# Kernel tuning notes

Measured on AMD Instinct MI355X. Metric: run time of the kernel, lower is better.

The kernel has to match this reference:

```python
import jax, jax.numpy as jnp
import numpy as np

B, N, D, H = 2, 2048, 2048, 16
HD = D // H  # head_dim = 128
EPS = 1e-06

def rmsnorm(x, w, eps=EPS):
    xf = x.astype(jnp.float32)
    y = xf * jax.lax.rsqrt(jnp.mean(xf * xf, axis=-1, keepdims=True) + eps)
    return y.astype(x.dtype) * w

def rope_apply(x, freqs, num_heads):
    # x: [B, S, D]; freqs: [S, 1, HD//2, 2] = (cos, sin) of complex rotation
    b, s, d = x.shape
    hd = d // num_heads
    xr = x.reshape(b, s, num_heads, hd // 2, 2)
    x0, x1 = xr[..., 0], xr[..., 1]
    fr, fi = freqs[..., 0], freqs[..., 1]  # broadcast [S,1,HD//2] over heads
    out = jnp.stack([x0 * fr - x1 * fi, x0 * fi + x1 * fr], axis=-1)
    return out.reshape(b, s, d).astype(x.dtype)

def attention(q, k, v, num_heads):
    b, s, d = q.shape
    hd = d // num_heads
    qh = q.reshape(b, s, num_heads, hd).transpose(0, 2, 1, 3)  # b h s d
    kh = k.reshape(b, s, num_heads, hd).transpose(0, 2, 1, 3)
    vh = v.reshape(b, s, num_heads, hd).transpose(0, 2, 1, 3)
    scale = hd ** -0.5
    scores = jnp.einsum('bhqd,bhkd->bhqk', qh, kh) * scale
    probs = jax.nn.softmax(scores, axis=-1)
    out = jnp.einsum('bhqk,bhkd->bhqd', probs, vh)
    return out.transpose(0, 2, 1, 3).reshape(b, s, d)

def setup_inputs() -> dict:
    key = jax.random.key(0)
    ks = jax.random.split(key, 8)
    x = jax.random.normal(ks[0], (B, N, D), jnp.float32)
    # standard RoPE frequencies
    pos = jnp.arange(N, dtype=jnp.float32)
    inv = 1.0 / (10000.0 ** (jnp.arange(0, HD, 2, dtype=jnp.float32) / HD))
    ang = pos[:, None] * inv[None, :]  # [N, HD//2]
    freqs = jnp.stack([jnp.cos(ang), jnp.sin(ang)], axis=-1)[:, None, :, :]  # [N,1,HD//2,2]
    s = 0.02
    wq = jax.random.normal(ks[1], (D, D), jnp.float32) * s
    wk = jax.random.normal(ks[2], (D, D), jnp.float32) * s
    wv = jax.random.normal(ks[3], (D, D), jnp.float32) * s
    wo = jax.random.normal(ks[4], (D, D), jnp.float32) * s
    bq = jnp.zeros((D,), jnp.float32)
    bk = jnp.zeros((D,), jnp.float32)
    bv = jnp.zeros((D,), jnp.float32)
    bo = jnp.zeros((D,), jnp.float32)
    gq = jnp.ones((D,), jnp.float32)
    gk = jnp.ones((D,), jnp.float32)
    return {"x": x, "freqs": freqs, "wq": wq, "bq": bq, "wk": wk, "bk": bk,
            "wv": wv, "bv": bv, "wo": wo, "bo": bo, "gq": gq, "gk": gk}

def reference(x, freqs, wq, bq, wk, bk, wv, bv, wo, bo, gq, gk):
    q = rmsnorm(x @ wq.T + bq, gq)
    k = rmsnorm(x @ wk.T + bk, gk)
    v = x @ wv.T + bv
    q = rope_apply(q, freqs, H)
    k = rope_apply(k, freqs, H)
    attn_out = attention(q, k, v, H)
    return attn_out @ wo.T + bo
```

## Files before the change

kernel.cpp:

```cpp
#include <hip/hip_runtime.h>
#include <hip/hip_bf16.h>
#include <stdint.h>


typedef __bf16 bf16;
typedef __bf16 bf16x8 __attribute__((ext_vector_type(8)));
typedef __bf16 bf16x4 __attribute__((ext_vector_type(4)));
typedef float  f32x4  __attribute__((ext_vector_type(4)));
typedef float  f32x16 __attribute__((ext_vector_type(16)));
typedef unsigned int uint2v __attribute__((ext_vector_type(2)));

#define MTOT   4096
#define DMODEL 2048
#define NSEQ   2048
#define NHEAD  16
#define HDIM   128

static __device__ __forceinline__ void async_ld16(const void* g, void* l) {
  void* gnc = const_cast<void*>(g);
  __builtin_amdgcn_global_load_lds((__attribute__((address_space(1))) void*)gnc,
                                   (__attribute__((address_space(3))) void*)l,
                                   16, 0, 0);
}

#define XG (MTOT * DMODEL / 8)
#define WG (DMODEL * DMODEL / 8)

__global__ __launch_bounds__(256) void k_cvt4(
    const float* __restrict__ x, const float* __restrict__ wq,
    const float* __restrict__ wk, const float* __restrict__ wv,
    bf16* __restrict__ xb, bf16* __restrict__ wqb, bf16* __restrict__ wkb,
    bf16* __restrict__ wvb) {
  int stride = gridDim.x * blockDim.x;
  for (int i = blockIdx.x * blockDim.x + threadIdx.x; i < XG + 3 * WG;
       i += stride) {
    const float* src;
    bf16* dst;
    int off;
    if (i < XG) { src = x; dst = xb; off = i; }
    else if (i < XG + WG) { src = wq; dst = wqb; off = i - XG; }
    else if (i < XG + 2 * WG) { src = wk; dst = wkb; off = i - XG - WG; }
    else { src = wv; dst = wvb; off = i - XG - 2 * WG; }
    const float4* p = (const float4*)(src) + 2 * (size_t)off;
    float4 a = p[0], b = p[1];
    bf16x8 o;
    o[0] = (bf16)a.x; o[1] = (bf16)a.y; o[2] = (bf16)a.z; o[3] = (bf16)a.w;
    o[4] = (bf16)b.x; o[5] = (bf16)b.y; o[6] = (bf16)b.z; o[7] = (bf16)b.w;
    *((bf16x8*)(dst) + off) = o;
  }
}

__global__ __launch_bounds__(256) void k_cvt(const float* __restrict__ in,
                                             bf16* __restrict__ out, int n8) {
  int stride = gridDim.x * blockDim.x;
  for (int i = blockIdx.x * blockDim.x + threadIdx.x; i < n8; i += stride) {
    const float4* p = (const float4*)(in) + 2 * (size_t)i;
    float4 a = p[0], b = p[1];
    bf16x8 o;
    o[0] = (bf16)a.x; o[1] = (bf16)a.y; o[2] = (bf16)a.z; o[3] = (bf16)a.w;
    o[4] = (bf16)b.x; o[5] = (bf16)b.y; o[6] = (bf16)b.z; o[7] = (bf16)b.w;
    *((bf16x8*)(out) + i) = o;
  }
}

__global__ __launch_bounds__(512, 2) void k_gemm_qk(
    const bf16* __restrict__ xb, const bf16* __restrict__ wq,
    const bf16* __restrict__ wk, const float* __restrict__ bq,
    const float* __restrict__ bk, bf16* __restrict__ q, bf16* __restrict__ k) {
  extern __shared__ __align__(16) bf16 dyn[];

  const int swz = (blockIdx.x & 7) * 32 + (blockIdx.x >> 3);
  const int mt = swz >> 4, nt = swz & 15;
  const int sec = nt >> 3;
  const int m0 = mt * 256, n0 = (nt & 7) * 256;
  const bf16* W = sec ? wk : wq;
  const float* bias = sec ? bk : bq;
  bf16* outp = sec ? k : q;

  const int tid = threadIdx.x;
  const int lane = tid & 63, w = tid >> 6;
  const int wm = w >> 2, wn = w & 3;
  const int g = lane >> 4, r0 = lane & 15;

  f32x4 acc[8][4];
  const f32x4 vzero = {0.f, 0.f, 0.f, 0.f};
#pragma unroll
  for (int i = 0; i < 8; ++i)
#pragma unroll
    for (int j = 0; j < 4; ++j) acc[i][j] = vzero;

  const bf16* Abase = xb + (size_t)m0 * DMODEL;
  const bf16* Wbase = W + (size_t)n0 * DMODEL;

  auto stage = [&](int kt, int buf) {
    const bf16* asrc = Abase + kt * 64;
    const bf16* bsrc = Wbase + kt * 64;
    bf16* sA = dyn + buf * 32768;
    bf16* sB = sA + 16384;
#pragma unroll
    for (int p = 0; p < 4; ++p) {
      int ch = tid + p * 512;
      int row = ch >> 3, c = (ch & 7) ^ (row & 7);
      async_ld16(asrc + (size_t)row * DMODEL + c * 8, sA + ch * 8);
    }
#pragma unroll
    for (int p = 0; p < 4; ++p) {
      int ch = tid + p * 512;
      int row = ch >> 3, c = (ch & 7) ^ (row & 7);
      async_ld16(bsrc + (size_t)row * DMODEL + c * 8, sB + ch * 8);
    }
  };

  const int NT = DMODEL / 64;
  stage(0, 0);
  for (int kt = 0; kt < NT; ++kt) {
    const int cur = kt & 1;
    if (kt > 0) __builtin_amdgcn_s_barrier();
    if (kt + 1 < NT) {
      stage(kt + 1, cur ^ 1);
      asm volatile("s_waitcnt vmcnt(8)" ::: "memory");
    } else {
      asm volatile("s_waitcnt vmcnt(0)" ::: "memory");
    }
    __builtin_amdgcn_s_barrier();
    const bf16* sA = dyn + cur * 32768;
    const bf16* sB = sA + 16384;

    bf16x8 a0[8], a1[8], b0[4], b1[4];
#pragma unroll
    for (int i = 0; i < 4; ++i) {
      int ra = wm * 128 + i * 16 + r0;
#pragma unroll
      for (int ks = 0; ks < 2; ++ks) {
        int cc = ks * 4 + g;
        a0[i * 2 + ks] = *(const bf16x8*)(sA + ra * 64 + ((cc ^ (ra & 7)) << 3));
      }
    }
#pragma unroll
    for (int j = 0; j < 2; ++j) {
      int rb = wn * 64 + j * 16 + r0;
#pragma unroll
      for (int ks = 0; ks < 2; ++ks) {
        int cc = ks * 4 + g;
        b0[j * 2 + ks] = *(const bf16x8*)(sB + rb * 64 + ((cc ^ (rb & 7)) << 3));
      }
    }
#pragma unroll
    for (int j = 0; j < 2; ++j) {
      int rb = wn * 64 + 32 + j * 16 + r0;
#pragma unroll
      for (int ks = 0; ks < 2; ++ks) {
        int cc = ks * 4 + g;
        b1[j * 2 + ks] = *(const bf16x8*)(sB + rb * 64 + ((cc ^ (rb & 7)) << 3));
      }
    }
    __builtin_amdgcn_s_setprio(1);
#pragma unroll
    for (int i = 0; i < 4; ++i)
#pragma unroll
      for (int j = 0; j < 2; ++j)
#pragma unroll
        for (int ks = 0; ks < 2; ++ks)
          acc[i][j] = __builtin_amdgcn_mfma_f32_16x16x32_bf16(
              a0[i * 2 + ks], b0[j * 2 + ks], acc[i][j], 0, 0, 0);
    __builtin_amdgcn_s_setprio(0);
#pragma unroll
    for (int i = 0; i < 4; ++i) {
      int ra = wm * 128 + 64 + i * 16 + r0;
#pragma unroll
      for (int ks = 0; ks < 2; ++ks) {
        int cc = ks * 4 + g;
        a1[i * 2 + ks] = *(const bf16x8*)(sA + ra * 64 + ((cc ^ (ra & 7)) << 3));
      }
    }
    __builtin_amdgcn_s_setprio(1);
#pragma unroll
    for (int i = 0; i < 4; ++i)
#pragma unroll
      for (int j = 0; j < 2; ++j)
#pragma unroll
        for (int ks = 0; ks < 2; ++ks)
          acc[i][2 + j] = __builtin_amdgcn_mfma_f32_16x16x32_bf16(
              a0[i * 2 + ks], b1[j * 2 + ks], acc[i][2 + j], 0, 0, 0);
    __builtin_amdgcn_s_setprio(0);
    __builtin_amdgcn_s_setprio(1);
#pragma unroll
    for (int i = 0; i < 4; ++i)
#pragma unroll
      for (int j = 0; j < 2; ++j)
#pragma unroll
        for (int ks = 0; ks < 2; ++ks)
          acc[4 + i][j] = __builtin_amdgcn_mfma_f32_16x16x32_bf16(
              a1[i * 2 + ks], b0[j * 2 + ks], acc[4 + i][j], 0, 0, 0);
    __builtin_amdgcn_s_setprio(0);
    __builtin_amdgcn_s_setprio(1);
#pragma unroll
    for (int i = 0; i < 4; ++i)
#pragma unroll
      for (int j = 0; j < 2; ++j)
#pragma unroll
        for (int ks = 0; ks < 2; ++ks)
          acc[4 + i][2 + j] = __builtin_amdgcn_mfma_f32_16x16x32_bf16(
              a1[i * 2 + ks], b1[j * 2 + ks], acc[4 + i][2 + j], 0, 0, 0);
    __builtin_amdgcn_s_setprio(0);
  }

#pragma unroll
  for (int i = 0; i < 8; ++i) {
#pragma unroll
    for (int j = 0; j < 4; ++j) {
      int mb = m0 + wm * 128 + (i >> 2) * 64 + (i & 3) * 16 + g * 4;
      int n = n0 + wn * 64 + (j >> 1) * 32 + (j & 1) * 16 + r0;
      float bn = bias[n];
#pragma unroll
      for (int r = 0; r < 4; ++r)
        outp[(size_t)(mb + r) * DMODEL + n] = (bf16)(acc[i][j][r] + bn);
    }
  }
}

#define BUFELEMS (384 * 64)

template <int OUTMODE>
static __device__ __forceinline__ void gemm256_body(
    const bf16* __restrict__ A, const bf16* __restrict__ W,
    const float* __restrict__ bias, void* __restrict__ outp, int m0, int n0) {
  extern __shared__ __align__(16) bf16 dynls[];

  const int tid = threadIdx.x;
  const int lane = tid & 63, w = tid >> 6;
  const int wm = w >> 2, wn = w & 3;
  const int g = lane >> 4, r0 = lane & 15;

  f32x4 acc[4][4];
  const f32x4 vzero = {0.f, 0.f, 0.f, 0.f};
#pragma unroll
  for (int i = 0; i < 4; ++i)
#pragma unroll
    for (int j = 0; j < 4; ++j) acc[i][j] = vzero;

  const bf16* Abase = A + (size_t)m0 * DMODEL;
  const bf16* Wbase = W + (size_t)n0 * DMODEL;

  auto stage_a = [&](int kt, int buf) {
    const bf16* asrc = Abase + kt * 64;
    const bf16* bsrc = Wbase + kt * 64;
    bf16* sBuf = dynls + buf * BUFELEMS;
#pragma unroll
    for (int p = 0; p < 2; ++p) {
      int ch = tid + p * 512;
      int row = ch >> 3, c = (ch & 7) ^ (row & 7);
      async_ld16(asrc + (size_t)row * DMODEL + c * 8, sBuf + ch * 8);
    }
    {
      int ch = tid;
      int row = ch >> 3, c = (ch & 7) ^ (row & 7);
      async_ld16(bsrc + (size_t)row * DMODEL + c * 8, sBuf + 128 * 64 + ch * 8);
    }
  };
  auto stage_b = [&](int kt, int buf) {
    const bf16* bsrc = Wbase + kt * 64;
    bf16* sBuf = dynls + buf * BUFELEMS + 128 * 64;
#pragma unroll
    for (int p = 1; p < 4; ++p) {
      int ch = tid + p * 512;
      int row = ch >> 3, c = (ch & 7) ^ (row & 7);
      async_ld16(bsrc + (size_t)row * DMODEL + c * 8, sBuf + ch * 8);
    }
  };

  const int NT = DMODEL / 64;
  stage_a(0, 0); stage_b(0, 0);
  stage_a(1, 1); stage_b(1, 1);
  asm volatile("s_waitcnt vmcnt(6)" ::: "memory");
  __builtin_amdgcn_s_barrier();

  for (int kt = 0; kt < NT; ++kt) {
    const bf16* sA = dynls + (kt % 3) * BUFELEMS;
    const bf16* sB = sA + 128 * 64;
    const bool pf = (kt + 2) < NT;
    const int nb = (kt + 2) % 3;

#pragma unroll
    for (int ks = 0; ks < 2; ++ks) {
      bf16x8 af[4], bfr[4];
      const int cc = ks * 4 + g;
#pragma unroll
      for (int i = 0; i < 4; ++i) {
        int ra = wm * 64 + i * 16 + r0;
        af[i] = *(const bf16x8*)(sA + ra * 64 + ((cc ^ (ra & 7)) << 3));
        int rb = wn * 64 + i * 16 + r0;
        bfr[i] = *(const bf16x8*)(sB + rb * 64 + ((cc ^ (rb & 7)) << 3));
      }
      if (ks == 0) {
        if (pf) stage_a(kt + 2, nb);
      } else {
        if (pf) {
          stage_b(kt + 2, nb);
          asm volatile("s_waitcnt vmcnt(6)" ::: "memory");
        } else {
          asm volatile("s_waitcnt vmcnt(0)" ::: "memory");
        }
      }
      __builtin_amdgcn_sched_barrier(0);
      __builtin_amdgcn_s_barrier();
      __builtin_amdgcn_sched_barrier(0);
      __builtin_amdgcn_s_setprio(1);
#pragma unroll
      for (int i = 0; i < 4; ++i)
#pragma unroll
        for (int j = 0; j < 4; ++j)
          acc[i][j] = __builtin_amdgcn_mfma_f32_16x16x32_bf16(af[i], bfr[j],
                                                              acc[i][j], 0, 0, 0);
      __builtin_amdgcn_s_setprio(0);
    }
  }

#pragma unroll
  for (int i = 0; i < 4; ++i) {
#pragma unroll
    for (int j = 0; j < 4; ++j) {
      int mb = m0 + wm * 64 + i * 16 + g * 4;
      int n = n0 + wn * 64 + j * 16 + r0;
      float bn = bias[n];
      if (OUTMODE == 0) {
        bf16* o = (bf16*)outp;
#pragma unroll
        for (int r = 0; r < 4; ++r)
          o[(size_t)(mb + r) * DMODEL + n] = (bf16)(acc[i][j][r] + bn);
      } else if (OUTMODE == 2) {
        float* o = (float*)outp;
#pragma unroll
        for (int r = 0; r < 4; ++r)
          o[(size_t)(mb + r) * DMODEL + n] = acc[i][j][r] + bn;
      } else {
        bf16* o = (bf16*)outp;
        int bb = mb >> 11, s = mb & (NSEQ - 1);
        bf16x4 pk;
#pragma unroll
        for (int r = 0; r < 4; ++r) pk[r] = (bf16)(acc[i][j][r] + bn);
        *(bf16x4*)(o + (size_t)(bb * DMODEL + n) * NSEQ + s) = pk;
      }
    }
  }
}

__global__ __launch_bounds__(512, 2) void k_gemm_v(
    const bf16* __restrict__ xb, const bf16* __restrict__ wv,
    const float* __restrict__ bv, bf16* __restrict__ vt) {
  gemm256_body<1>(xb, wv, bv, vt, blockIdx.y * 128, blockIdx.x * 256);
}

__global__ __launch_bounds__(512, 2) void k_gemm_out(
    const bf16* __restrict__ ab, const bf16* __restrict__ wo,
    const float* __restrict__ bo, float* __restrict__ out) {
  gemm256_body<2>(ab, wo, bo, out, blockIdx.y * 128, blockIdx.x * 256);
}

__global__ __launch_bounds__(256) void k_norm_rope(
    bf16* __restrict__ q, bf16* __restrict__ kk, const float* __restrict__ gq,
    const float* __restrict__ gk, const float* __restrict__ freqs) {
  int bidx = blockIdx.x;
  bf16* buf = (bidx < MTOT) ? q : kk;
  const float* gw = (bidx < MTOT) ? gq : gk;
  float qs = (bidx < MTOT) ? 0.08838834764831845f : 1.0f;
  int row = bidx & (MTOT - 1);
  int s = row & (NSEQ - 1);
  int tid = threadIdx.x;
  int i0 = tid * 8;
  bf16* ptr = buf + (size_t)row * DMODEL + i0;
  bf16x8 v = *(const bf16x8*)ptr;
  float x[8];
  float ssq = 0.f;
#pragma unroll
  for (int j = 0; j < 8; ++j) {
    x[j] = (float)v[j];
    ssq += x[j] * x[j];
  }
#pragma unroll
  for (int off = 1; off < 64; off <<= 1) ssq += __shfl_xor(ssq, off);
  __shared__ float part[4];
  if ((tid & 63) == 0) part[tid >> 6] = ssq;
  __syncthreads();
  float tot = part[0] + part[1] + part[2] + part[3];
  float sc = rsqrtf(tot * (1.f / DMODEL) + 1e-6f) * qs;
  float4 g0 = *(const float4*)(gw + i0);
  float4 g1 = *(const float4*)(gw + i0 + 4);
  float y[8];
  y[0] = x[0] * sc * g0.x; y[1] = x[1] * sc * g0.y;
  y[2] = x[2] * sc * g0.z; y[3] = x[3] * sc * g0.w;
  y[4] = x[4] * sc * g1.x; y[5] = x[5] * sc * g1.y;
  y[6] = x[6] * sc * g1.z; y[7] = x[7] * sc * g1.w;
  int dl = i0 & (HDIM - 1);
  const float* fp = freqs + (size_t)s * HDIM + dl;
  float4 f0 = *(const float4*)fp;
  float4 f1 = *(const float4*)(fp + 4);
  bf16x8 out;
  out[0] = (bf16)(y[0] * f0.x - y[1] * f0.y);
  out[1] = (bf16)(y[0] * f0.y + y[1] * f0.x);
  out[2] = (bf16)(y[2] * f0.z - y[3] * f0.w);
  out[3] = (bf16)(y[2] * f0.w + y[3] * f0.z);
  out[4] = (bf16)(y[4] * f1.x - y[5] * f1.y);
  out[5] = (bf16)(y[4] * f1.y + y[5] * f1.x);
  out[6] = (bf16)(y[6] * f1.z - y[7] * f1.w);
  out[7] = (bf16)(y[6] * f1.w + y[7] * f1.z);
  *(bf16x8*)ptr = out;
}

__global__ __launch_bounds__(256, 2) void k_attn(const bf16* __restrict__ q,
                                                 const bf16* __restrict__ k,
                                                 const bf16* __restrict__ vt,
                                                 bf16* __restrict__ o) {
  __shared__ __align__(16) bf16 sk[2][64 * 128];
  __shared__ __align__(16) bf16 sv[2][128 * 64];
  const int bid = blockIdx.x;
  const int idx = bid >> 3;
  const int bh = (bid & 7) * 4 + (idx >> 4);
  const int qt = idx & 15;
  const int bb = bh >> 4, h = bh & 15;
  const int tid = threadIdx.x;
  const int lane = tid & 63, w = tid >> 6;
  const int l31 = lane & 31, b5 = lane >> 5;

  bf16x8 qf[8];
  {
    const bf16* qb =
        q + (size_t)(bb * NSEQ + qt * 128 + w * 32 + l31) * DMODEL + h * HDIM +
        b5 * 8;
#pragma unroll
    for (int kk = 0; kk < 8; ++kk) qf[kk] = *(const bf16x8*)(qb + kk * 16);
  }

  f32x16 oacc[4];
#pragma unroll
  for (int dt = 0; dt < 4; ++dt)
#pragma unroll
    for (int r = 0; r < 16; ++r) oacc[dt][r] = 0.f;
  float m = -3.0e38f, l = 0.f;

  const bf16* kbase = k + (size_t)(bb * NSEQ) * DMODEL + h * HDIM;
  const bf16* vbase = vt + (size_t)(bb * DMODEL + h * HDIM) * NSEQ;

  auto stage = [&](int t, int buf) {
    int k0 = t * 64;
#pragma unroll
    for (int p = 0; p < 4; ++p) {
      int ch = tid + p * 256;
      int row = ch >> 4, cs = ch & 15;
      int c = cs ^ (row & 7);
      async_ld16(kbase + (size_t)(k0 + row) * DMODEL + c * 8, &sk[buf][ch * 8]);
    }
#pragma unroll
    for (int p = 0; p < 4; ++p) {
      int ch = tid + p * 256;
      int row = ch >> 3, cs = ch & 7;
      int c = cs ^ (row & 7);
      async_ld16(vbase + (size_t)row * NSEQ + k0 + c * 8, &sv[buf][ch * 8]);
    }
  };

  stage(0, 0);
  for (int t = 0; t < NSEQ / 64; ++t) {
    const int cur = t & 1;
    asm volatile("s_waitcnt vmcnt(0)" ::: "memory");
    __syncthreads();
    if (t + 1 < NSEQ / 64) stage(t + 1, cur ^ 1);

    f32x16 sacc[2];
#pragma unroll
    for (int s = 0; s < 2; ++s)
#pragma unroll
      for (int r = 0; r < 16; ++r) sacc[s][r] = 0.f;
#pragma unroll
    for (int s = 0; s < 2; ++s) {
      const int row = s * 32 + l31;
#pragma unroll
      for (int kk = 0; kk < 8; ++kk) {
        const int c = 2 * kk + b5;
        bf16x8 kf = *(const bf16x8*)(&sk[cur][row * 128 + ((c ^ (row & 7)) << 3)]);
        sacc[s] = __builtin_amdgcn_mfma_f32_32x32x16_bf16(kf, qf[kk], sacc[s],
                                                          0, 0, 0);
      }
    }

    float t1[8];
#pragma unroll
    for (int i = 0; i < 8; ++i)
      t1[i] = fmaxf(fmaxf(sacc[0][2 * i], sacc[0][2 * i + 1]),
                    fmaxf(sacc[1][2 * i], sacc[1][2 * i + 1]));
    float pm = fmaxf(fmaxf(fmaxf(t1[0], t1[1]), fmaxf(t1[2], t1[3])),
                     fmaxf(fmaxf(t1[4], t1[5]), fmaxf(t1[6], t1[7])));
    {
      uint2v r2 = __builtin_amdgcn_permlane32_swap(__float_as_uint(pm),
                                                   __float_as_uint(pm), false,
                                                   false);
      pm = fmaxf(__uint_as_float(r2.x), __uint_as_float(r2.y));
    }
    const int need = __any(pm > m + 8.0f);
    if (need) {
      float mn = fmaxf(m, pm);
      float alpha = __expf(m - mn);
      m = mn;
      l *= alpha;
#pragma unroll
      for (int dt = 0; dt < 4; ++dt)
#pragma unroll
        for (int r = 0; r < 16; ++r) oacc[dt][r] *= alpha;
    }

    float rs = 0.f;
#pragma unroll
    for (int s = 0; s < 2; ++s)
#pragma unroll
      for (int r = 0; r < 16; ++r) {
        float pv = __expf(sacc[s][r] - m);
        sacc[s][r] = pv;
        rs += pv;
      }
    {
      uint2v r2 = __builtin_amdgcn_permlane32_swap(__float_as_uint(rs),
                                                   __float_as_uint(rs), false,
                                                   false);
      rs = __uint_as_float(r2.x) + __uint_as_float(r2.y);
    }
    l += rs;

    uint32_t P2[16];
#pragma unroll
    for (int s = 0; s < 2; ++s)
#pragma unroll
      for (int i = 0; i < 8; ++i)
        asm("v_cvt_pk_bf16_f32 %0, %1, %2"
            : "=v"(P2[s * 8 + i])
            : "v"(sacc[s][2 * i]), "v"(sacc[s][2 * i + 1]));

#pragma unroll
    for (int s = 0; s < 2; ++s) {
#pragma unroll
      for (int u = 0; u < 2; ++u) {
        union { uint32_t uw[4]; bf16x8 v; } pb;
        uint2v ra = __builtin_amdgcn_permlane32_swap(P2[s * 8 + 4 * u],
                                                     P2[s * 8 + 4 * u + 2],
                                                     false, false);
        uint2v rb = __builtin_amdgcn_permlane32_swap(P2[s * 8 + 4 * u + 1],
                                                     P2[s * 8 + 4 * u + 3],
                                                     false, false);
        pb.uw[0] = ra.x;
        pb.uw[1] = rb.x;
        pb.uw[2] = ra.y;
        pb.uw[3] = rb.y;
        const int c = 4 * s + 2 * u + b5;
#pragma unroll
        for (int dt = 0; dt < 4; ++dt) {
          const int rv = dt * 32 + l31;
          bf16x8 vf =
              *(const bf16x8*)(&sv[cur][rv * 64 + ((c ^ (rv & 7)) << 3)]);
          oacc[dt] = __builtin_amdgcn_mfma_f32_32x32x16_bf16(vf, pb.v, oacc[dt],
                                                             0, 0, 0);
        }
      }
    }
  }

  const float rl = 1.f / l;
  bf16* ob = o + (size_t)(bb * NSEQ + qt * 128 + w * 32 + l31) * DMODEL +
             h * HDIM;
#pragma unroll
  for (int dt = 0; dt < 4; ++dt) {
#pragma unroll
    for (int rg = 0; rg < 4; ++rg) {
      bf16x4 pk4;
#pragma unroll
      for (int e = 0; e < 4; ++e) pk4[e] = (bf16)(oacc[dt][rg * 4 + e] * rl);
      *(bf16x4*)(ob + dt * 32 + rg * 8 + b5 * 4) = pk4;
    }
  }
}

extern "C" void kernel_launch(void* const* d_in, const int* in_sizes, int n_in,
                              void* d_out, int out_size, void* d_ws,
                              size_t ws_size, hipStream_t stream) {
  (void)in_sizes; (void)n_in; (void)out_size; (void)ws_size;
  const float* x = (const float*)d_in[0];
  const float* freqs = (const float*)d_in[1];
  const float* wq = (const float*)d_in[2];
  const float* bq = (const float*)d_in[3];
  const float* wk = (const float*)d_in[4];
  const float* bk = (const float*)d_in[5];
  const float* wv = (const float*)d_in[6];
  const float* bv = (const float*)d_in[7];
  const float* wo = (const float*)d_in[8];
  const float* bo = (const float*)d_in[9];
  const float* gq = (const float*)d_in[10];
  const float* gk = (const float*)d_in[11];

  char* ws = (char*)d_ws;
  const size_t SZ_TOK = (size_t)MTOT * DMODEL * sizeof(bf16);
  const size_t SZ_W = (size_t)DMODEL * DMODEL * sizeof(bf16);
  bf16* xb = (bf16*)ws;
  bf16* qb = (bf16*)(ws + SZ_TOK);
  bf16* kb = (bf16*)(ws + 2 * SZ_TOK);
  bf16* vtb = (bf16*)(ws + 3 * SZ_TOK);
  bf16* wqb = (bf16*)(ws + 4 * SZ_TOK);
  bf16* wkb = (bf16*)(ws + 4 * SZ_TOK + SZ_W);
  bf16* wvb = (bf16*)(ws + 4 * SZ_TOK + 2 * SZ_W);

  const int LDSB = 3 * BUFELEMS * (int)sizeof(bf16);
  const int LDSQK = 2 * 32768 * (int)sizeof(bf16);
  hipFuncSetAttribute((const void*)k_gemm_qk,
                      hipFuncAttributeMaxDynamicSharedMemorySize, LDSQK);
  hipFuncSetAttribute((const void*)k_gemm_v,
                      hipFuncAttributeMaxDynamicSharedMemorySize, LDSB);
  hipFuncSetAttribute((const void*)k_gemm_out,
                      hipFuncAttributeMaxDynamicSharedMemorySize, LDSB);

  k_cvt4<<<2048, 256, 0, stream>>>(x, wq, wk, wv, xb, wqb, wkb, wvb);

  k_gemm_qk<<<256, 512, LDSQK, stream>>>(xb, wqb, wkb, bq, bk, qb, kb);
  k_gemm_v<<<dim3(8, 32), 512, LDSB, stream>>>(xb, wvb, bv, vtb);

  k_cvt<<<1024, 256, 0, stream>>>(wo, wqb, (DMODEL * DMODEL) / 8);

  k_norm_rope<<<2 * MTOT, 256, 0, stream>>>(qb, kb, gq, gk, freqs);

  k_attn<<<512, 256, 0, stream>>>(qb, kb, vtb, xb);

  k_gemm_out<<<dim3(8, 32), 512, LDSB, stream>>>(xb, wqb, bo, (float*)d_out);
}
```

Measured before the change: 263.3 us.

## Process two query sub-tiles per warp in attention and use exp2 softmax

Each attention warp now handles 64 query rows (two 32-row sub-tiles) instead of 32, so every K/V fragment loaded from LDS feeds two MFMAs. The block count drops from 512 to 256 and occupancy is lowered to one block per CU to make room for the doubled accumulators. The softmax now works in base 2: log2(e) is folded into the Q scale in the norm/rope kernel, the hardware v_exp_f32 is used, and the running max is subtracted by seeding the score accumulators with -m. Rescaling only happens when the max exceeds a fixed threshold. The costs are higher register pressure, fewer waves to hide latency, and with 256 blocks only about one block per CU.

```diff
diff --git a/kernel.cpp b/kernel.cpp
--- a/kernel.cpp
+++ b/kernel.cpp
@@ -21,6 +21,12 @@
   __builtin_amdgcn_global_load_lds((__attribute__((address_space(1))) void*)gnc,
                                    (__attribute__((address_space(3))) void*)l,
                                    16, 0, 0);
+}
+
+static __device__ __forceinline__ float exp2_hw(float x) {
+  float r;
+  asm("v_exp_f32 %0, %1" : "=v"(r) : "v"(x));
+  return r;
 }
 
 #define XG (MTOT * DMODEL / 8)
@@ -363,7 +369,8 @@
   int bidx = blockIdx.x;
   bf16* buf = (bidx < MTOT) ? q : kk;
   const float* gw = (bidx < MTOT) ? gq : gk;
-  float qs = (bidx < MTOT) ? 0.08838834764831845f : 1.0f;
+  float qs = (bidx < MTOT) ? (0.08838834764831845f * 1.4426950408889634f)
+                           : 1.0f;
   int row = bidx & (MTOT - 1);
   int s = row & (NSEQ - 1);
   int tid = threadIdx.x;
@@ -407,7 +414,9 @@
   *(bf16x8*)ptr = out;
 }
 
-__global__ __launch_bounds__(256, 2) void k_attn(const bf16* __restrict__ q,
+#define LOG2E_THR 11.541560327111707f
+
+__global__ __launch_bounds__(256, 1) void k_attn(const bf16* __restrict__ q,
                                                  const bf16* __restrict__ k,
                                                  const bf16* __restrict__ vt,
                                                  bf16* __restrict__ o) {
@@ -415,28 +424,32 @@
   __shared__ __align__(16) bf16 sv[2][128 * 64];
   const int bid = blockIdx.x;
   const int idx = bid >> 3;
-  const int bh = (bid & 7) * 4 + (idx >> 4);
-  const int qt = idx & 15;
+  const int bh = (bid & 7) * 4 + (idx >> 3);
+  const int qt = idx & 7;
   const int bb = bh >> 4, h = bh & 15;
   const int tid = threadIdx.x;
   const int lane = tid & 63, w = tid >> 6;
   const int l31 = lane & 31, b5 = lane >> 5;
 
-  bf16x8 qf[8];
+  bf16x8 qfA[8], qfB[8];
   {
-    const bf16* qb =
-        q + (size_t)(bb * NSEQ + qt * 128 + w * 32 + l31) * DMODEL + h * HDIM +
+    const bf16* qbA =
+        q + (size_t)(bb * NSEQ + qt * 256 + w * 64 + l31) * DMODEL + h * HDIM +
         b5 * 8;
-#pragma unroll
-    for (int kk = 0; kk < 8; ++kk) qf[kk] = *(const bf16x8*)(qb + kk * 16);
-  }
-
-  f32x16 oacc[4];
+    const bf16* qbB = qbA + (size_t)32 * DMODEL;
+#pragma unroll
+    for (int kk = 0; kk < 8; ++kk) {
+      qfA[kk] = *(const bf16x8*)(qbA + kk * 16);
+      qfB[kk] = *(const bf16x8*)(qbB + kk * 16);
+    }
+  }
+
+  f32x16 oaccA[4], oaccB[4];
 #pragma unroll
   for (int dt = 0; dt < 4; ++dt)
 #pragma unroll
-    for (int r = 0; r < 16; ++r) oacc[dt][r] = 0.f;
-  float m = -3.0e38f, l = 0.f;
+    for (int r = 0; r < 16; ++r) { oaccA[dt][r] = 0.f; oaccB[dt][r] = 0.f; }
+  float mA = 0.f, lA = 0.f, mB = 0.f, lB = 0.f;
 
   const bf16* kbase = k + (size_t)(bb * NSEQ) * DMODEL + h * HDIM;
   const bf16* vbase = vt + (size_t)(bb * DMODEL + h * HDIM) * NSEQ;
@@ -466,11 +479,11 @@
     __syncthreads();
     if (t + 1 < NSEQ / 64) stage(t + 1, cur ^ 1);
 
-    f32x16 sacc[2];
+    f32x16 saccA[2], saccB[2];
 #pragma unroll
     for (int s = 0; s < 2; ++s)
 #pragma unroll
-      for (int r = 0; r < 16; ++r) sacc[s][r] = 0.f;
+      for (int r = 0; r < 16; ++r) { saccA[s][r] = -mA; saccB[s][r] = -mB; }
 #pragma unroll
     for (int s = 0; s < 2; ++s) {
       const int row = s * 32 + l31;
@@ -478,101 +491,159 @@
       for (int kk = 0; kk < 8; ++kk) {
         const int c = 2 * kk + b5;
         bf16x8 kf = *(const bf16x8*)(&sk[cur][row * 128 + ((c ^ (row & 7)) << 3)]);
-        sacc[s] = __builtin_amdgcn_mfma_f32_32x32x16_bf16(kf, qf[kk], sacc[s],
-                                                          0, 0, 0);
-      }
-    }
-
-    float t1[8];
-#pragma unroll
-    for (int i = 0; i < 8; ++i)
-      t1[i] = fmaxf(fmaxf(sacc[0][2 * i], sacc[0][2 * i + 1]),
-                    fmaxf(sacc[1][2 * i], sacc[1][2 * i + 1]));
-    float pm = fmaxf(fmaxf(fmaxf(t1[0], t1[1]), fmaxf(t1[2], t1[3])),
-                     fmaxf(fmaxf(t1[4], t1[5]), fmaxf(t1[6], t1[7])));
+        saccA[s] = __builtin_amdgcn_mfma_f32_32x32x16_bf16(kf, qfA[kk],
+                                                           saccA[s], 0, 0, 0);
+        saccB[s] = __builtin_amdgcn_mfma_f32_32x32x16_bf16(kf, qfB[kk],
+                                                           saccB[s], 0, 0, 0);
+      }
+    }
+
+    uint32_t P2A[16], P2B[16];
     {
+      float t1[8];
+#pragma unroll
+      for (int i = 0; i < 8; ++i)
+        t1[i] = fmaxf(fmaxf(saccA[0][2 * i], saccA[0][2 * i + 1]),
+                      fmaxf(saccA[1][2 * i], saccA[1][2 * i + 1]));
+      float pm = fmaxf(fmaxf(fmaxf(t1[0], t1[1]), fmaxf(t1[2], t1[3])),
+                       fmaxf(fmaxf(t1[4], t1[5]), fmaxf(t1[6], t1[7])));
       uint2v r2 = __builtin_amdgcn_permlane32_swap(__float_as_uint(pm),
                                                    __float_as_uint(pm), false,
                                                    false);
       pm = fmaxf(__uint_as_float(r2.x), __uint_as_float(r2.y));
-    }
-    const int need = __any(pm > m + 8.0f);
-    if (need) {
-      float mn = fmaxf(m, pm);
-      float alpha = __expf(m - mn);
-      m = mn;
-      l *= alpha;
-#pragma unroll
-      for (int dt = 0; dt < 4; ++dt)
-#pragma unroll
-        for (int r = 0; r < 16; ++r) oacc[dt][r] *= alpha;
-    }
-
-    float rs = 0.f;
-#pragma unroll
-    for (int s = 0; s < 2; ++s)
-#pragma unroll
-      for (int r = 0; r < 16; ++r) {
-        float pv = __expf(sacc[s][r] - m);
-        sacc[s][r] = pv;
-        rs += pv;
-      }
-    {
-      uint2v r2 = __builtin_amdgcn_permlane32_swap(__float_as_uint(rs),
+      if (__any(pm > LOG2E_THR)) {
+        float d = fmaxf(pm, 0.f);
+        mA += d;
+        float alpha = exp2_hw(-d);
+        lA *= alpha;
+#pragma unroll
+        for (int dt = 0; dt < 4; ++dt)
+#pragma unroll
+          for (int r = 0; r < 16; ++r) oaccA[dt][r] *= alpha;
+#pragma unroll
+        for (int s = 0; s < 2; ++s)
+#pragma unroll
+          for (int r = 0; r < 16; ++r) saccA[s][r] -= d;
+      }
+      float rs = 0.f;
+#pragma unroll
+      for (int s = 0; s < 2; ++s)
+#pragma unroll
+        for (int r = 0; r < 16; ++r) {
+          float pv = exp2_hw(saccA[s][r]);
+          saccA[s][r] = pv;
+          rs += pv;
+        }
+      uint2v r3 = __builtin_amdgcn_permlane32_swap(__float_as_uint(rs),
                                                    __float_as_uint(rs), false,
                                                    false);
-      rs = __uint_as_float(r2.x) + __uint_as_float(r2.y);
-    }
-    l += rs;
-
-    uint32_t P2[16];
-#pragma unroll
-    for (int s = 0; s < 2; ++s)
+      lA += __uint_as_float(r3.x) + __uint_as_float(r3.y);
+#pragma unroll
+      for (int s = 0; s < 2; ++s)
+#pragma unroll
+        for (int i = 0; i < 8; ++i)
+          asm("v_cvt_pk_bf16_f32 %0, %1, %2"
+              : "=v"(P2A[s * 8 + i])
+              : "v"(saccA[s][2 * i]), "v"(saccA[s][2 * i + 1]));
+    }
+    {
+      float t1[8];
 #pragma unroll
       for (int i = 0; i < 8; ++i)
-        asm("v_cvt_pk_bf16_f32 %0, %1, %2"
-            : "=v"(P2[s * 8 + i])
-            : "v"(sacc[s][2 * i]), "v"(sacc[s][2 * i + 1]));
+        t1[i] = fmaxf(fmaxf(saccB[0][2 * i], saccB[0][2 * i + 1]),
+                      fmaxf(saccB[1][2 * i], saccB[1][2 * i + 1]));
+      float pm = fmaxf(fmaxf(fmaxf(t1[0], t1[1]), fmaxf(t1[2], t1[3])),
+                       fmaxf(fmaxf(t1[4], t1[5]), fmaxf(t1[6], t1[7])));
+      uint2v r2 = __builtin_amdgcn_permlane32_swap(__float_as_uint(pm),
+                                                   __float_as_uint(pm), false,
+                                                   false);
+      pm = fmaxf(__uint_as_float(r2.x), __uint_as_float(r2.y));
+      if (__any(pm > LOG2E_THR)) {
+        float d = fmaxf(pm, 0.f);
+        mB += d;
+        float alpha = exp2_hw(-d);
+        lB *= alpha;
+#pragma unroll
+        for (int dt = 0; dt < 4; ++dt)
+#pragma unroll
+          for (int r = 0; r < 16; ++r) oaccB[dt][r] *= alpha;
+#pragma unroll
+        for (int s = 0; s < 2; ++s)
+#pragma unroll
+          for (int r = 0; r < 16; ++r) saccB[s][r] -= d;
+      }
+      float rs = 0.f;
+#pragma unroll
+      for (int s = 0; s < 2; ++s)
+#pragma unroll
+        for (int r = 0; r < 16; ++r) {
+          float pv = exp2_hw(saccB[s][r]);
+          saccB[s][r] = pv;
+          rs += pv;
+        }
+      uint2v r3 = __builtin_amdgcn_permlane32_swap(__float_as_uint(rs),
+                                                   __float_as_uint(rs), false,
+                                                   false);
+      lB += __uint_as_float(r3.x) + __uint_as_float(r3.y);
+#pragma unroll
+      for (int s = 0; s < 2; ++s)
+#pragma unroll
+        for (int i = 0; i < 8; ++i)
+          asm("v_cvt_pk_bf16_f32 %0, %1, %2"
+              : "=v"(P2B[s * 8 + i])
+              : "v"(saccB[s][2 * i]), "v"(saccB[s][2 * i + 1]));
+    }
 
 #pragma unroll
     for (int s = 0; s < 2; ++s) {
 #pragma unroll
       for (int u = 0; u < 2; ++u) {
-        union { uint32_t uw[4]; bf16x8 v; } pb;
-        uint2v ra = __builtin_amdgcn_permlane32_swap(P2[s * 8 + 4 * u],
-                                                     P2[s * 8 + 4 * u + 2],
+        union { uint32_t uw[4]; bf16x8 v; } pbA, pbB;
+        uint2v ra = __builtin_amdgcn_permlane32_swap(P2A[s * 8 + 4 * u],
+                                                     P2A[s * 8 + 4 * u + 2],
                                                      false, false);
-        uint2v rb = __builtin_amdgcn_permlane32_swap(P2[s * 8 + 4 * u + 1],
-                                                     P2[s * 8 + 4 * u + 3],
+        uint2v rb = __builtin_amdgcn_permlane32_swap(P2A[s * 8 + 4 * u + 1],
+                                                     P2A[s * 8 + 4 * u + 3],
                                                      false, false);
-        pb.uw[0] = ra.x;
-        pb.uw[1] = rb.x;
-        pb.uw[2] = ra.y;
-        pb.uw[3] = rb.y;
+        pbA.uw[0] = ra.x; pbA.uw[1] = rb.x; pbA.uw[2] = ra.y; pbA.uw[3] = rb.y;
+        uint2v rc = __builtin_amdgcn_permlane32_swap(P2B[s * 8 + 4 * u],
+                                                     P2B[s * 8 + 4 * u + 2],
+                                                     false, false);
+        uint2v rd = __builtin_amdgcn_permlane32_swap(P2B[s * 8 + 4 * u + 1],
+                                                     P2B[s * 8 + 4 * u + 3],
+                                                     false, false);
+        pbB.uw[0] = rc.x; pbB.uw[1] = rd.x; pbB.uw[2] = rc.y; pbB.uw[3] = rd.y;
         const int c = 4 * s + 2 * u + b5;
 #pragma unroll
         for (int dt = 0; dt < 4; ++dt) {
           const int rv = dt * 32 + l31;
           bf16x8 vf =
               *(const bf16x8*)(&sv[cur][rv * 64 + ((c ^ (rv & 7)) << 3)]);
-          oacc[dt] = __builtin_amdgcn_mfma_f32_32x32x16_bf16(vf, pb.v, oacc[dt],
-                                                             0, 0, 0);
+          oaccA[dt] = __builtin_amdgcn_mfma_f32_32x32x16_bf16(vf, pbA.v,
+                                                              oaccA[dt], 0, 0, 0);
+          oaccB[dt] = __builtin_amdgcn_mfma_f32_32x32x16_bf16(vf, pbB.v,
+                                                              oaccB[dt], 0, 0, 0);
         }
       }
     }
   }
 
-  const float rl = 1.f / l;
-  bf16* ob = o + (size_t)(bb * NSEQ + qt * 128 + w * 32 + l31) * DMODEL +
-             h * HDIM;
+  const float rlA = 1.f / lA, rlB = 1.f / lB;
+  bf16* obA = o + (size_t)(bb * NSEQ + qt * 256 + w * 64 + l31) * DMODEL +
+              h * HDIM;
+  bf16* obB = obA + (size_t)32 * DMODEL;
 #pragma unroll
   for (int dt = 0; dt < 4; ++dt) {
 #pragma unroll
     for (int rg = 0; rg < 4; ++rg) {
-      bf16x4 pk4;
-#pragma unroll
-      for (int e = 0; e < 4; ++e) pk4[e] = (bf16)(oacc[dt][rg * 4 + e] * rl);
-      *(bf16x4*)(ob + dt * 32 + rg * 8 + b5 * 4) = pk4;
+      bf16x4 pk4, pk5;
+#pragma unroll
+      for (int e = 0; e < 4; ++e) {
+        pk4[e] = (bf16)(oaccA[dt][rg * 4 + e] * rlA);
+        pk5[e] = (bf16)(oaccB[dt][rg * 4 + e] * rlB);
+      }
+      *(bf16x4*)(obA + dt * 32 + rg * 8 + b5 * 4) = pk4;
+      *(bf16x4*)(obB + dt * 32 + rg * 8 + b5 * 4) = pk5;
     }
   }
 }
@@ -623,7 +694,7 @@
 
   k_norm_rope<<<2 * MTOT, 256, 0, stream>>>(qb, kb, gq, gk, freqs);
 
-  k_attn<<<512, 256, 0, stream>>>(qb, kb, vtb, xb);
+  k_attn<<<256, 256, 0, stream>>>(qb, kb, vtb, xb);
 
   k_gemm_out<<<dim3(8, 32), 512, LDSB, stream>>>(xb, wqb, bo, (float*)d_out);
 }
```

New measurement: 285.2 us. 1.08x slower.

## Use exp2 with log2e-folded Q scale, max-offset MFMA init, setprio and wider K swizzle

Applied to the files above, without the earlier changes.

Folds log2(e) into the query scale so the attention softmax can use the raw v_exp_f32 (exp2) instruction instead of __expf. It also initialises the score accumulators with -m so the max subtraction is absorbed into the MFMA, and rescales lazily against a threshold expressed in log2 units. It wraps the MFMA sections in s_setprio to favour matrix issue across waves, and widens the K LDS swizzle from 3 to 4 bits to reduce bank conflicts. The risks are numerical: the starting max is now 0 instead of -inf, and the lazy threshold bounds overflow only for moderate score ranges.

```diff
diff --git a/kernel.cpp b/kernel.cpp
--- a/kernel.cpp
+++ b/kernel.cpp
@@ -21,6 +21,12 @@
   __builtin_amdgcn_global_load_lds((__attribute__((address_space(1))) void*)gnc,
                                    (__attribute__((address_space(3))) void*)l,
                                    16, 0, 0);
+}
+
+static __device__ __forceinline__ float exp2_hw(float x) {
+  float r;
+  asm("v_exp_f32 %0, %1" : "=v"(r) : "v"(x));
+  return r;
 }
 
 #define XG (MTOT * DMODEL / 8)
@@ -363,7 +369,8 @@
   int bidx = blockIdx.x;
   bf16* buf = (bidx < MTOT) ? q : kk;
   const float* gw = (bidx < MTOT) ? gq : gk;
-  float qs = (bidx < MTOT) ? 0.08838834764831845f : 1.0f;
+  float qs = (bidx < MTOT) ? (0.08838834764831845f * 1.4426950408889634f)
+                           : 1.0f;
   int row = bidx & (MTOT - 1);
   int s = row & (NSEQ - 1);
   int tid = threadIdx.x;
@@ -407,6 +414,8 @@
   *(bf16x8*)ptr = out;
 }
 
+#define LOG2E_THR 11.541560327111707f
+
 __global__ __launch_bounds__(256, 2) void k_attn(const bf16* __restrict__ q,
                                                  const bf16* __restrict__ k,
                                                  const bf16* __restrict__ vt,
@@ -436,7 +445,7 @@
   for (int dt = 0; dt < 4; ++dt)
 #pragma unroll
     for (int r = 0; r < 16; ++r) oacc[dt][r] = 0.f;
-  float m = -3.0e38f, l = 0.f;
+  float m = 0.f, l = 0.f;
 
   const bf16* kbase = k + (size_t)(bb * NSEQ) * DMODEL + h * HDIM;
   const bf16* vbase = vt + (size_t)(bb * DMODEL + h * HDIM) * NSEQ;
@@ -447,7 +456,7 @@
     for (int p = 0; p < 4; ++p) {
       int ch = tid + p * 256;
       int row = ch >> 4, cs = ch & 15;
-      int c = cs ^ (row & 7);
+      int c = cs ^ (row & 15);
       async_ld16(kbase + (size_t)(k0 + row) * DMODEL + c * 8, &sk[buf][ch * 8]);
     }
 #pragma unroll
@@ -470,18 +479,20 @@
 #pragma unroll
     for (int s = 0; s < 2; ++s)
 #pragma unroll
-      for (int r = 0; r < 16; ++r) sacc[s][r] = 0.f;
+      for (int r = 0; r < 16; ++r) sacc[s][r] = -m;
+    __builtin_amdgcn_s_setprio(1);
 #pragma unroll
     for (int s = 0; s < 2; ++s) {
       const int row = s * 32 + l31;
 #pragma unroll
       for (int kk = 0; kk < 8; ++kk) {
         const int c = 2 * kk + b5;
-        bf16x8 kf = *(const bf16x8*)(&sk[cur][row * 128 + ((c ^ (row & 7)) << 3)]);
+        bf16x8 kf = *(const bf16x8*)(&sk[cur][row * 128 + ((c ^ (row & 15)) << 3)]);
         sacc[s] = __builtin_amdgcn_mfma_f32_32x32x16_bf16(kf, qf[kk], sacc[s],
                                                           0, 0, 0);
       }
     }
+    __builtin_amdgcn_s_setprio(0);
 
     float t1[8];
 #pragma unroll
@@ -496,16 +507,19 @@
                                                    false);
       pm = fmaxf(__uint_as_float(r2.x), __uint_as_float(r2.y));
     }
-    const int need = __any(pm > m + 8.0f);
-    if (need) {
-      float mn = fmaxf(m, pm);
-      float alpha = __expf(m - mn);
-      m = mn;
+    if (__any(pm > LOG2E_THR)) {
+      float d = fmaxf(pm, 0.f);
+      m += d;
+      float alpha = exp2_hw(-d);
       l *= alpha;
 #pragma unroll
       for (int dt = 0; dt < 4; ++dt)
 #pragma unroll
         for (int r = 0; r < 16; ++r) oacc[dt][r] *= alpha;
+#pragma unroll
+      for (int s = 0; s < 2; ++s)
+#pragma unroll
+        for (int r = 0; r < 16; ++r) sacc[s][r] -= d;
     }
 
     float rs = 0.f;
@@ -513,7 +527,7 @@
     for (int s = 0; s < 2; ++s)
 #pragma unroll
       for (int r = 0; r < 16; ++r) {
-        float pv = __expf(sacc[s][r] - m);
+        float pv = exp2_hw(sacc[s][r]);
         sacc[s][r] = pv;
         rs += pv;
       }
@@ -534,6 +548,7 @@
             : "=v"(P2[s * 8 + i])
             : "v"(sacc[s][2 * i]), "v"(sacc[s][2 * i + 1]));
 
+    __builtin_amdgcn_s_setprio(1);
 #pragma unroll
     for (int s = 0; s < 2; ++s) {
 #pragma unroll
@@ -560,6 +575,7 @@
         }
       }
     }
+    __builtin_amdgcn_s_setprio(0);
   }
 
   const float rl = 1.f / l;
```

New measurement: 258.1 us. About the same (-2.0%).
